# Optimization experiments

Measured on AMD Instinct MI355X. Metric: run time of the kernel, lower is better.

The kernel has to match this reference:

```python
import jax, jax.numpy as jnp
import numpy as np

N = 100000   # nodes
E = 1600000  # edges (avg degree 16)
F_IN = 50    # dataset.num_features
C = 32       # dataset.num_classes == hidden == out channels


def setup_inputs() -> dict:
    key = jax.random.key(0)
    ks = jax.random.split(key, 12)
    x = jax.random.normal(ks[0], (N, F_IN), dtype=jnp.float32)
    edge_index = jax.random.randint(ks[1], (2, E), 0, N, dtype=jnp.int64)
    dims = [(F_IN, C), (C, C), (C, C)]
    inp = {"x": x, "edge_index": edge_index}
    for i, (din, dout) in enumerate(dims, start=1):
        s = 1.0 / np.sqrt(din)
        inp[f"Wl{i}"] = jax.random.uniform(ks[2 + 3 * (i - 1)], (din, dout), jnp.float32, -s, s)
        inp[f"bl{i}"] = jax.random.uniform(ks[3 + 3 * (i - 1)], (dout,), jnp.float32, -s, s)
        inp[f"Wr{i}"] = jax.random.uniform(ks[4 + 3 * (i - 1)], (din, dout), jnp.float32, -s, s)
    return inp


def _sage_conv(x, src, dst, Wl, bl, Wr):
    # message = x[src]; scatter-max into dst; lin_l(agg) + lin_r(x)
    msg = x[src]                                      # [E, d_in]
    agg = jax.ops.segment_max(msg, dst, num_segments=N)
    agg = jnp.where(jnp.isfinite(agg), agg, jnp.zeros((), agg.dtype))  # empty segments -> 0
    return agg @ Wl + bl + x @ Wr


def reference(x, edge_index, Wl1, bl1, Wr1, Wl2, bl2, Wr2, Wl3, bl3, Wr3):
    src, dst = edge_index[0], edge_index[1]
    h = jax.nn.relu(_sage_conv(x, src, dst, Wl1, bl1, Wr1))
    h = jax.nn.relu(_sage_conv(h, src, dst, Wl2, bl2, Wr2))
    h = _sage_conv(h, src, dst, Wl3, bl3, Wr3)
    return jax.nn.log_softmax(h, axis=1)
```

## Files before the change

### kernel.cpp

```cpp
#include <hip/hip_runtime.h>
#include <math.h>

#define NN 100000
#define CD 32
#define NPB 4

#define B1N ((NN + 255) >> 8)
#define EPB_A 2048

typedef unsigned int   uint32;
typedef unsigned short ushort16;

__device__ __forceinline__ ushort16 f2b(float f) {
    uint32 u = __float_as_uint(f);
    u = (u + 0x7FFFu + ((u >> 16) & 1u)) >> 16;
    return (ushort16)u;
}
__device__ __forceinline__ float b2f_lo(uint32 u) { return __uint_as_float(u << 16); }
__device__ __forceinline__ float b2f_hi(uint32 u) { return __uint_as_float(u & 0xFFFF0000u); }

__device__ __forceinline__ uint32 pkmax(uint32 a, uint32 b) {
    uint32 d;
    asm("v_pk_max_u16 %0, %1, %2" : "=v"(d) : "v"(a), "v"(b));
    return d;
}
__device__ __forceinline__ uint32 key16(float f) {
    uint32 b = (uint32)f2b(f);
    return b ^ ((__float_as_uint(f) >> 31) ? 0xFFFFu : 0x8000u);
}
__device__ __forceinline__ uint32 dec_pk(uint32 k) {
    uint32 m = (~k >> 15) & 0x00010001u;
    uint32 X = 0x80008000u | ((m << 15) - m);
    return k ^ X;
}

__device__ __forceinline__ int edge_is64(const void* edge) {
    const long long* p = (const long long*)edge;
    int lane = threadIdx.x & 63;
    int bad = 0;
    for (int i = lane; i < 512; i += 64) {
        long long v = p[i];
        if (v < 0 || v >= NN) bad = 1;
    }
    unsigned long long anybad = __ballot(bad);
    return (anybad == 0ULL) ? 1 : 0;
}

__device__ __forceinline__ int load_idx(const void* edge, int i, int is64) {
    if (is64) return (int)((const long long*)edge)[i];
    return ((const int*)edge)[i];
}

__global__ __launch_bounds__(256) void cvt_hist_kernel(const float* __restrict__ x,
                                                       uint32* __restrict__ xb,
                                                       const void* edge, int E,
                                                       int* __restrict__ hist,
                                                       int nblkA) {
    __shared__ int lh[B1N];
    const int t = threadIdx.x;
    if ((int)blockIdx.x < nblkA) {
        const int is64 = edge_is64(edge);
        for (int b = t; b < B1N; b += 256) lh[b] = 0;
        __syncthreads();
        const int e0 = blockIdx.x * EPB_A + t;
#pragma unroll
        for (int k = 0; k < 8; ++k) {
            int e = e0 + k * 256;
            if (e < E) {
                int d = load_idx(edge, E + e, is64);
                atomicAdd(&lh[d >> 8], 1);
            }
        }
        __syncthreads();
        int* gh = hist + (size_t)blockIdx.x * B1N;
        for (int b = t; b < B1N; b += 256) gh[b] = lh[b];
    } else {
        const int tt = (blockIdx.x - nblkA) * 256 + t;
        if (tt >= NN * 32) return;
        const int n = tt >> 5;
        const int c = tt & 31;
        if (c >= 25) { xb[tt] = 0; return; }
        float2 v = *(const float2*)&x[n * 50 + 2 * c];
        xb[tt] = key16(v.x) | (key16(v.y) << 16);
    }
}

__global__ __launch_bounds__(256) void scanA_kernel(int* __restrict__ hist,
                                                    int nblk,
                                                    int* __restrict__ binTotal) {
    __shared__ int ts[256];
    const int bin = blockIdx.x;
    const int t = threadIdx.x;
    const int base = t * 4;
    int v0 = (base + 0 < nblk) ? hist[(size_t)(base + 0) * B1N + bin] : 0;
    int v1 = (base + 1 < nblk) ? hist[(size_t)(base + 1) * B1N + bin] : 0;
    int v2 = (base + 2 < nblk) ? hist[(size_t)(base + 2) * B1N + bin] : 0;
    int v3 = (base + 3 < nblk) ? hist[(size_t)(base + 3) * B1N + bin] : 0;
    const int s = v0 + v1 + v2 + v3;
    ts[t] = s;
    __syncthreads();
    for (int off = 1; off < 256; off <<= 1) {
        int u = (t >= off) ? ts[t - off] : 0;
        __syncthreads();
        ts[t] += u;
        __syncthreads();
    }
    int e = ts[t] - s;
    if (base + 0 < nblk) { hist[(size_t)(base + 0) * B1N + bin] = e; e += v0; }
    if (base + 1 < nblk) { hist[(size_t)(base + 1) * B1N + bin] = e; e += v1; }
    if (base + 2 < nblk) { hist[(size_t)(base + 2) * B1N + bin] = e; e += v2; }
    if (base + 3 < nblk) { hist[(size_t)(base + 3) * B1N + bin] = e; e += v3; }
    if (t == 255) binTotal[bin] = ts[255];
}

__device__ __forceinline__ void scan_bins_lds(const int* __restrict__ binTotal,
                                              int* ts, int* lbase) {
    const int t = threadIdx.x;
    const int base = t * 2;
    const int v0 = (base + 0 < B1N) ? binTotal[base + 0] : 0;
    const int v1 = (base + 1 < B1N) ? binTotal[base + 1] : 0;
    const int s = v0 + v1;
    ts[t] = s;
    __syncthreads();
    for (int off = 1; off < 256; off <<= 1) {
        int u = (t >= off) ? ts[t - off] : 0;
        __syncthreads();
        ts[t] += u;
        __syncthreads();
    }
    const int e = ts[t] - s;
    if (base + 0 < B1N) lbase[base + 0] = e;
    if (base + 1 < B1N) lbase[base + 1] = e + v0;
    if (t == 255) lbase[B1N] = ts[255];
    __syncthreads();
}

__global__ __launch_bounds__(256) void scatter_kernel(const void* edge, int E,
                                                      const int* __restrict__ hist,
                                                      const int* __restrict__ binTotal,
                                                      uint32* __restrict__ bucketed) {
    __shared__ int ts[256];
    __shared__ int lbase[B1N + 1];
    __shared__ int cur[B1N];
    const int is64 = edge_is64(edge);
    const int t = threadIdx.x;
    scan_bins_lds(binTotal, ts, lbase);
    const int* gh = hist + (size_t)blockIdx.x * B1N;
    for (int b = t; b < B1N; b += 256) cur[b] = lbase[b] + gh[b];
    __syncthreads();
    const int e0 = blockIdx.x * EPB_A + t;
#pragma unroll
    for (int k = 0; k < 8; ++k) {
        int e = e0 + k * 256;
        if (e < E) {
            int s = load_idx(edge, e, is64);
            int d = load_idx(edge, E + e, is64);
            int pos = atomicAdd(&cur[d >> 8], 1);
            bucketed[pos] = (uint32)s | ((uint32)(d & 255) << 17);
        }
    }
}

__global__ __launch_bounds__(256) void bucket_kernel(const uint32* __restrict__ bucketed,
                                                     const int* __restrict__ binTotal,
                                                     int* __restrict__ offsets,
                                                     int* __restrict__ csr_src) {
    __shared__ int ts[256];
    __shared__ int lbase[B1N + 1];
    __shared__ int h[256];
    __shared__ int sc[256];
    __shared__ int cur[256];
    const int bkt = blockIdx.x;
    const int t = threadIdx.x;
    scan_bins_lds(binTotal, ts, lbase);
    const int start = lbase[bkt];
    const int end   = lbase[bkt + 1];
    h[t] = 0;
    __syncthreads();
    for (int i = start + t; i < end; i += 256)
        atomicAdd(&h[bucketed[i] >> 17], 1);
    __syncthreads();
    const int v = h[t];
    sc[t] = v;
    __syncthreads();
    for (int off = 1; off < 256; off <<= 1) {
        int u = (t >= off) ? sc[t - off] : 0;
        __syncthreads();
        sc[t] += u;
        __syncthreads();
    }
    const int excl = sc[t] - v;
    const int node = bkt * 256 + t;
    if (node < NN) offsets[node] = start + excl;
    cur[t] = start + excl;
    __syncthreads();
    for (int i = start + t; i < end; i += 256) {
        uint32 p = bucketed[i];
        int pos = atomicAdd(&cur[p >> 17], 1);
        csr_src[pos] = (int)(p & 0x1FFFFu);
    }
    if (bkt == B1N - 1 && t == 0) offsets[NN] = end;
}


__global__ void gather50_kernel(const uint32* __restrict__ hb,
                                const int* __restrict__ offsets,
                                const int* __restrict__ csr_src,
                                uint32* __restrict__ aggB) {
    const int tid  = threadIdx.x;
    const int g    = tid >> 6;
    const int lane = tid & 63;
    const int p    = lane >> 5;
    const int j    = lane & 31;
    const int n    = blockIdx.x * NPB + g;
    if (n >= NN) return;

    const int beg = offsets[n];
    const int end = offsets[n + 1];
    const char* hbase = (const char*)hb;
    const uint32 joff = (uint32)(j << 2);
    const int lb = p << 5;

    uint32 a_[8];
#pragma unroll
    for (int k = 0; k < 8; ++k) a_[k] = 0;

    for (int ib = beg; ib < end; ib += 64) {
        const int rem = end - ib;
        const int mm  = rem < 64 ? rem : 64;
        const int myidx = 2 * j + p;
        int sidx = 0;
        if (myidx < mm) sidx = csr_src[ib + myidx];
        int k = p;
        for (; k + 14 < mm; k += 16) {
            const int kh = lb + (k >> 1);
#pragma unroll
            for (int kk = 0; kk < 8; ++kk) {
                int s = __shfl(sidx, kh + kk);
                uint32 u = *(const uint32*)(hbase + ((((uint32)s) << 7) | joff));
                a_[kk] = pkmax(a_[kk], u);
            }
        }
        for (; k + 6 < mm; k += 8) {
            const int kh = lb + (k >> 1);
#pragma unroll
            for (int kk = 0; kk < 4; ++kk) {
                int s = __shfl(sidx, kh + kk);
                uint32 u = *(const uint32*)(hbase + ((((uint32)s) << 7) | joff));
                a_[kk] = pkmax(a_[kk], u);
            }
        }
        for (; k < mm; k += 2) {
            int s = __shfl(sidx, lb + (k >> 1));
            uint32 u = *(const uint32*)(hbase + ((((uint32)s) << 7) | joff));
            a_[0] = pkmax(a_[0], u);
        }
    }
#pragma unroll
    for (int off2 = 4; off2 > 0; off2 >>= 1)
#pragma unroll
        for (int k = 0; k < off2; ++k)
            a_[k] = pkmax(a_[k], a_[k + off2]);
    uint32 r = a_[0];
    r = pkmax(r, (uint32)__shfl_xor((int)r, 32));
    if (p == 0 && j < 25) {
        aggB[(size_t)n * 32 + j] = (beg == end) ? 0x80008000u : r;
    }
}

__global__ void gather32_kernel(const uint32* __restrict__ hb,
                                const int* __restrict__ offsets,
                                const int* __restrict__ csr_src,
                                uint32* __restrict__ aggB) {
    const int tid  = threadIdx.x;
    const int g    = tid >> 6;
    const int lane = tid & 63;
    const int e    = lane >> 4;
    const int c    = lane & 15;
    const int n    = blockIdx.x * NPB + g;
    if (n >= NN) return;

    const int beg = offsets[n];
    const int end = offsets[n + 1];
    const char* hbase = (const char*)hb;
    const uint32 coff = (uint32)(c << 2);
    const int lb = e << 4;

    uint32 a0 = 0, a1 = 0, a2 = 0, a3 = 0;

    for (int ib = beg; ib < end; ib += 64) {
        const int rem = end - ib;
        const int mm  = rem < 64 ? rem : 64;
        const int myidx = 4 * c + e;
        int sidx = 0;
        if (myidx < mm) sidx = csr_src[ib + myidx];
        int k = e;
        for (; k + 12 < mm; k += 16) {
            const int m = lb + (k >> 2);
            int s0 = __shfl(sidx, m);
            int s1 = __shfl(sidx, m + 1);
            int s2 = __shfl(sidx, m + 2);
            int s3 = __shfl(sidx, m + 3);
            uint32 u0 = *(const uint32*)(hbase + ((((uint32)s0) << 6) | coff));
            uint32 u1 = *(const uint32*)(hbase + ((((uint32)s1) << 6) | coff));
            uint32 u2 = *(const uint32*)(hbase + ((((uint32)s2) << 6) | coff));
            uint32 u3 = *(const uint32*)(hbase + ((((uint32)s3) << 6) | coff));
            a0 = pkmax(a0, u0); a1 = pkmax(a1, u1);
            a2 = pkmax(a2, u2); a3 = pkmax(a3, u3);
        }
        for (; k < mm; k += 4) {
            int s = __shfl(sidx, lb + (k >> 2));
            uint32 u = *(const uint32*)(hbase + ((((uint32)s) << 6) | coff));
            a0 = pkmax(a0, u);
        }
    }
    uint32 r = pkmax(pkmax(a0, a1), pkmax(a2, a3));
    r = pkmax(r, (uint32)__shfl_xor((int)r, 16));
    r = pkmax(r, (uint32)__shfl_xor((int)r, 32));
    if (lane < 16) {
        aggB[(size_t)n * 16 + lane] = (beg == end) ? 0x80008000u : r;
    }
}

template <int DIN, int ASTR, int HSTR, int OSTR, int MODE>
__global__ void dense_kernel(const uint32* __restrict__ aggB,
                             const uint32* __restrict__ hB,
                             const float* __restrict__ Wl,
                             const float* __restrict__ bl,
                             const float* __restrict__ Wr,
                             void* __restrict__ out_v) {
    const int n = blockIdx.x * blockDim.x + threadIdx.x;
    if (n >= NN) return;

    float acc[CD];
#pragma unroll
    for (int j = 0; j < CD; ++j) acc[j] = bl[j];

    {
        const uint32* row = aggB + (size_t)n * ASTR;
        for (int c = 0; c < DIN / 4; ++c) {
            uint2 u = *(const uint2*)&row[c * 2];
            u.x = dec_pk(u.x); u.y = dec_pk(u.y);
            float d0 = b2f_lo(u.x), d1 = b2f_hi(u.x);
            float d2 = b2f_lo(u.y), d3 = b2f_hi(u.y);
            const float* w = Wl + c * 4 * CD;
#pragma unroll
            for (int j = 0; j < CD; ++j)
                acc[j] += d0 * w[j] + d1 * w[CD + j] + d2 * w[2 * CD + j] + d3 * w[3 * CD + j];
        }
        if (DIN % 4) {
            uint32 u = dec_pk(row[(DIN / 4) * 2]);
            float d0 = b2f_lo(u), d1 = b2f_hi(u);
            const float* w = Wl + (DIN - 2) * CD;
#pragma unroll
            for (int j = 0; j < CD; ++j)
                acc[j] += d0 * w[j] + d1 * w[CD + j];
        }
    }
    {
        const uint32* row = hB + (size_t)n * HSTR;
        for (int c = 0; c < DIN / 4; ++c) {
            uint2 u = *(const uint2*)&row[c * 2];
            u.x = dec_pk(u.x); u.y = dec_pk(u.y);
            float d0 = b2f_lo(u.x), d1 = b2f_hi(u.x);
            float d2 = b2f_lo(u.y), d3 = b2f_hi(u.y);
            const float* w = Wr + c * 4 * CD;
#pragma unroll
            for (int j = 0; j < CD; ++j)
                acc[j] += d0 * w[j] + d1 * w[CD + j] + d2 * w[2 * CD + j] + d3 * w[3 * CD + j];
        }
        if (DIN % 4) {
            uint32 u = dec_pk(row[(DIN / 4) * 2]);
            float d0 = b2f_lo(u), d1 = b2f_hi(u);
            const float* w = Wr + (DIN - 2) * CD;
#pragma unroll
            for (int j = 0; j < CD; ++j)
                acc[j] += d0 * w[j] + d1 * w[CD + j];
        }
    }

    if (MODE == 0) {
        uint32* orow = (uint32*)out_v + (size_t)n * OSTR;
#pragma unroll
        for (int c = 0; c < CD / 2; ++c) {
            float a0 = fmaxf(acc[2 * c],     0.0f);
            float a1 = fmaxf(acc[2 * c + 1], 0.0f);
            orow[c] = ((uint32)f2b(a0) | ((uint32)f2b(a1) << 16)) | 0x80008000u;
        }
    } else {
        float m = acc[0];
#pragma unroll
        for (int j = 1; j < CD; ++j) m = fmaxf(m, acc[j]);
        float s = 0.0f;
#pragma unroll
        for (int j = 0; j < CD; ++j) s += expf(acc[j] - m);
        const float lse = m + logf(s);
        float* orow = (float*)out_v + (size_t)n * CD;
#pragma unroll
        for (int j = 0; j < CD; ++j) orow[j] = acc[j] - lse;
    }
}

extern "C" void kernel_launch(void* const* d_in, const int* in_sizes, int n_in,
                              void* d_out, int out_size, void* d_ws, size_t ws_size,
                              hipStream_t stream) {
    const float* x    = (const float*)d_in[0];
    const void*  edge = d_in[1];
    const float* Wl1 = (const float*)d_in[2];
    const float* bl1 = (const float*)d_in[3];
    const float* Wr1 = (const float*)d_in[4];
    const float* Wl2 = (const float*)d_in[5];
    const float* bl2 = (const float*)d_in[6];
    const float* Wr2 = (const float*)d_in[7];
    const float* Wl3 = (const float*)d_in[8];
    const float* bl3 = (const float*)d_in[9];
    const float* Wr3 = (const float*)d_in[10];

    const int E = in_sizes[1] / 2;

    char* ws = (char*)d_ws;
    size_t off = 0;
    auto carve = [&](size_t bytes) {
        void* p = ws + off;
        off = (off + bytes + 255) & ~(size_t)255;
        return p;
    };
    int*    offsets   = (int*)   carve((size_t)(NN + 1) * 4);
    int*    binTotal  = (int*)   carve((size_t)B1N * 4);
    int*    csr_src   = (int*)   carve((size_t)E * 4);
    uint32* xb        = (uint32*)carve((size_t)NN * 32 * 4);
    uint32* h1b       = (uint32*)carve((size_t)NN * 16 * 4);
    (void)ws_size; (void)n_in; (void)out_size;

    uint32* bucketed = (uint32*)d_out;
    int*    hist     = (int*)((char*)d_out + (((size_t)E * 4 + 255) & ~(size_t)255));
    uint32* agg1 = (uint32*)d_out;
    uint32* agg2 = (uint32*)d_out;
    uint32* h2b  = xb;
    uint32* agg3 = h1b;

    const int nblkA = (E + EPB_A - 1) / EPB_A;
    const int cvtb  = (NN * 32 + 255) / 256;
    cvt_hist_kernel<<<nblkA + cvtb, 256, 0, stream>>>(x, xb, edge, E, hist, nblkA);
    scanA_kernel<<<B1N, 256, 0, stream>>>(hist, nblkA, binTotal);
    scatter_kernel<<<nblkA, 256, 0, stream>>>(edge, E, hist, binTotal, bucketed);
    bucket_kernel<<<B1N, 256, 0, stream>>>(bucketed, binTotal, offsets, csr_src);

    const int gb = (NN + NPB - 1) / NPB;
    const int db = (NN + 255) / 256;

    gather50_kernel<<<gb, 256, 0, stream>>>(xb, offsets, csr_src, agg1);
    dense_kernel<50, 32, 32, 16, 0><<<db, 256, 0, stream>>>(agg1, xb, Wl1, bl1, Wr1, h1b);
    gather32_kernel<<<gb, 256, 0, stream>>>(h1b, offsets, csr_src, agg2);
    dense_kernel<32, 16, 16, 16, 0><<<db, 256, 0, stream>>>(agg2, h1b, Wl2, bl2, Wr2, h2b);
    gather32_kernel<<<gb, 256, 0, stream>>>(h2b, offsets, csr_src, agg3);
    dense_kernel<32, 16, 16, 0, 2><<<db, 256, 0, stream>>>(agg3, h2b, Wl3, bl3, Wr3, d_out);
}
```

Baseline: 302.7 us.

## Split layer-1 features into column-partitioned tables and batch nodes per wave in gathers

The 50-wide bf16 input is repacked into three 16-column planes plus a separate 2-column tail. Layer-1 gather runs in three passes, one per plane, each reading 32-byte rows so a pass's table is smaller and caches better. A new dense50 kernel reads the split layout. Both gather kernels now process four nodes per wave with their index loads issued up front, giving more memory-level parallelism. The cost is more launched blocks and more register use per wave.

```diff
diff --git a/kernel.cpp b/kernel.cpp
--- a/kernel.cpp
+++ b/kernel.cpp
@@ -4,6 +4,8 @@
 #define NN 100000
 #define CD 32
 #define NPB 4
+#define G50_NPW 4
+#define G32_NPW 4
 
 #define B1N ((NN + 255) >> 8)
 #define EPB_A 2048
@@ -52,7 +54,8 @@
 }
 
 __global__ __launch_bounds__(256) void cvt_hist_kernel(const float* __restrict__ x,
-                                                       uint32* __restrict__ xb,
+                                                       uint32* __restrict__ xc,
+                                                       uint32* __restrict__ xc3,
                                                        const void* edge, int E,
                                                        int* __restrict__ hist,
                                                        int nblkA) {
@@ -76,12 +79,19 @@
         for (int b = t; b < B1N; b += 256) gh[b] = lh[b];
     } else {
         const int tt = (blockIdx.x - nblkA) * 256 + t;
-        if (tt >= NN * 32) return;
-        const int n = tt >> 5;
-        const int c = tt & 31;
-        if (c >= 25) { xb[tt] = 0; return; }
-        float2 v = *(const float2*)&x[n * 50 + 2 * c];
-        xb[tt] = key16(v.x) | (key16(v.y) << 16);
+        if (tt < NN * 24) {
+            const int p  = tt / (NN * 8);
+            const int r  = tt - p * NN * 8;
+            const int n  = r >> 3;
+            const int cc = r & 7;
+            const int u  = 8 * p + cc;
+            float2 v = *(const float2*)&x[n * 50 + 2 * u];
+            xc[tt] = key16(v.x) | (key16(v.y) << 16);
+        } else if (tt < NN * 24 + NN) {
+            const int n = tt - NN * 24;
+            float2 v = *(const float2*)&x[n * 50 + 48];
+            xc3[n] = key16(v.x) | (key16(v.y) << 16);
+        }
     }
 }
 
@@ -203,68 +213,113 @@
 }
 
 
-__global__ void gather50_kernel(const uint32* __restrict__ hb,
+__global__ void gather50_kernel(const uint32* __restrict__ xc,
+                                const uint32* __restrict__ xc3,
                                 const int* __restrict__ offsets,
                                 const int* __restrict__ csr_src,
-                                uint32* __restrict__ aggB) {
+                                uint32* __restrict__ aggp,
+                                uint32* __restrict__ agg24,
+                                int gb) {
     const int tid  = threadIdx.x;
     const int g    = tid >> 6;
     const int lane = tid & 63;
-    const int p    = lane >> 5;
-    const int j    = lane & 31;
-    const int n    = blockIdx.x * NPB + g;
-    if (n >= NN) return;
-
-    const int beg = offsets[n];
-    const int end = offsets[n + 1];
-    const char* hbase = (const char*)hb;
-    const uint32 joff = (uint32)(j << 2);
-    const int lb = p << 5;
-
-    uint32 a_[8];
-#pragma unroll
-    for (int k = 0; k < 8; ++k) a_[k] = 0;
-
-    for (int ib = beg; ib < end; ib += 64) {
-        const int rem = end - ib;
-        const int mm  = rem < 64 ? rem : 64;
-        const int myidx = 2 * j + p;
-        int sidx = 0;
-        if (myidx < mm) sidx = csr_src[ib + myidx];
-        int k = p;
-        for (; k + 14 < mm; k += 16) {
-            const int kh = lb + (k >> 1);
-#pragma unroll
-            for (int kk = 0; kk < 8; ++kk) {
-                int s = __shfl(sidx, kh + kk);
-                uint32 u = *(const uint32*)(hbase + ((((uint32)s) << 7) | joff));
-                a_[kk] = pkmax(a_[kk], u);
+    const int e    = lane & 7;
+    const int c    = lane >> 3;
+    const int pass = blockIdx.x / gb;
+    const int blk  = blockIdx.x - pass * gb;
+    const int n0   = (blk * NPB + g) * G50_NPW;
+    if (n0 >= NN) return;
+    const bool p0 = (pass == 0);
+
+    const char* tb = (const char*)(xc + (size_t)pass * NN * 8);
+    const uint32 coff = (uint32)(c << 2);
+
+    int beg[G50_NPW], end[G50_NPW], mm[G50_NPW], sidx[G50_NPW];
+#pragma unroll
+    for (int q = 0; q < G50_NPW; ++q) {
+        const int n = n0 + q;
+        const bool ok = (n < NN);
+        beg[q] = ok ? offsets[n] : 0;
+        end[q] = ok ? offsets[n + 1] : 0;
+        int d = end[q] - beg[q];
+        mm[q] = d < 64 ? d : 64;
+    }
+#pragma unroll
+    for (int q = 0; q < G50_NPW; ++q)
+        sidx[q] = (lane < mm[q]) ? csr_src[beg[q] + lane] : 0;
+
+    uint32 acc[G50_NPW], a24[G50_NPW];
+#pragma unroll
+    for (int q = 0; q < G50_NPW; ++q) { acc[q] = 0; a24[q] = 0; }
+
+#pragma unroll
+    for (int q = 0; q < G50_NPW; ++q) {
+        for (int k = e; k < mm[q]; k += 8) {
+            int s = __shfl(sidx[q], k);
+            acc[q] = pkmax(acc[q], *(const uint32*)(tb + ((((uint32)s) << 5) | coff)));
+        }
+        if (p0 && lane < mm[q]) a24[q] = pkmax(a24[q], xc3[sidx[q]]);
+    }
+#pragma unroll
+    for (int q = 0; q < G50_NPW; ++q) {
+        for (int ib = beg[q] + 64; ib < end[q]; ib += 64) {
+            const int rem = end[q] - ib;
+            const int m = rem < 64 ? rem : 64;
+            int sx = (lane < m) ? csr_src[ib + lane] : 0;
+            for (int k = e; k < m; k += 8) {
+                int s = __shfl(sx, k);
+                acc[q] = pkmax(acc[q], *(const uint32*)(tb + ((((uint32)s) << 5) | coff)));
             }
-        }
-        for (; k + 6 < mm; k += 8) {
-            const int kh = lb + (k >> 1);
-#pragma unroll
-            for (int kk = 0; kk < 4; ++kk) {
-                int s = __shfl(sidx, kh + kk);
-                uint32 u = *(const uint32*)(hbase + ((((uint32)s) << 7) | joff));
-                a_[kk] = pkmax(a_[kk], u);
-            }
-        }
-        for (; k < mm; k += 2) {
-            int s = __shfl(sidx, lb + (k >> 1));
-            uint32 u = *(const uint32*)(hbase + ((((uint32)s) << 7) | joff));
-            a_[0] = pkmax(a_[0], u);
-        }
-    }
-#pragma unroll
-    for (int off2 = 4; off2 > 0; off2 >>= 1)
-#pragma unroll
-        for (int k = 0; k < off2; ++k)
-            a_[k] = pkmax(a_[k], a_[k + off2]);
-    uint32 r = a_[0];
-    r = pkmax(r, (uint32)__shfl_xor((int)r, 32));
-    if (p == 0 && j < 25) {
-        aggB[(size_t)n * 32 + j] = (beg == end) ? 0x80008000u : r;
+            if (p0 && lane < m) a24[q] = pkmax(a24[q], xc3[sx]);
+        }
+    }
+
+#pragma unroll
+    for (int q = 0; q < G50_NPW; ++q) {
+        const int n = n0 + q;
+        uint32 r = acc[q];
+        r = pkmax(r, (uint32)__shfl_xor((int)r, 1));
+        r = pkmax(r, (uint32)__shfl_xor((int)r, 2));
+        r = pkmax(r, (uint32)__shfl_xor((int)r, 4));
+        if (e == 0 && n < NN) {
+            aggp[((size_t)pass * NN + n) * 8 + c] =
+                (beg[q] == end[q]) ? 0x80008000u : r;
+        }
+        if (p0) {
+            uint32 s24 = a24[q];
+            s24 = pkmax(s24, (uint32)__shfl_xor((int)s24, 1));
+            s24 = pkmax(s24, (uint32)__shfl_xor((int)s24, 2));
+            s24 = pkmax(s24, (uint32)__shfl_xor((int)s24, 4));
+            s24 = pkmax(s24, (uint32)__shfl_xor((int)s24, 8));
+            s24 = pkmax(s24, (uint32)__shfl_xor((int)s24, 16));
+            s24 = pkmax(s24, (uint32)__shfl_xor((int)s24, 32));
+            if (lane == 0 && n < NN)
+                agg24[n] = (beg[q] == end[q]) ? 0x80008000u : s24;
+        }
+    }
+}
+
+__device__ __forceinline__ void g32_window(uint32* a_, int sidx, int mm,
+                                           const char* hbase, uint32 coff,
+                                           int e, int lb) {
+    int k = e;
+    for (; k + 12 < mm; k += 16) {
+        const int m = lb + (k >> 2);
+        int s0 = __shfl(sidx, m);
+        int s1 = __shfl(sidx, m + 1);
+        int s2 = __shfl(sidx, m + 2);
+        int s3 = __shfl(sidx, m + 3);
+        uint32 u0 = *(const uint32*)(hbase + ((((uint32)s0) << 6) | coff));
+        uint32 u1 = *(const uint32*)(hbase + ((((uint32)s1) << 6) | coff));
+        uint32 u2 = *(const uint32*)(hbase + ((((uint32)s2) << 6) | coff));
+        uint32 u3 = *(const uint32*)(hbase + ((((uint32)s3) << 6) | coff));
+        a_[0] = pkmax(a_[0], u0); a_[1] = pkmax(a_[1], u1);
+        a_[2] = pkmax(a_[2], u2); a_[3] = pkmax(a_[3], u3);
+    }
+    for (; k < mm; k += 4) {
+        int s = __shfl(sidx, lb + (k >> 2));
+        uint32 u = *(const uint32*)(hbase + ((((uint32)s) << 6) | coff));
+        a_[0] = pkmax(a_[0], u);
     }
 }
 
@@ -277,48 +332,109 @@
     const int lane = tid & 63;
     const int e    = lane >> 4;
     const int c    = lane & 15;
-    const int n    = blockIdx.x * NPB + g;
-    if (n >= NN) return;
-
-    const int beg = offsets[n];
-    const int end = offsets[n + 1];
+    const int n0   = (blockIdx.x * NPB + g) * G32_NPW;
+    if (n0 >= NN) return;
+
     const char* hbase = (const char*)hb;
     const uint32 coff = (uint32)(c << 2);
     const int lb = e << 4;
-
-    uint32 a0 = 0, a1 = 0, a2 = 0, a3 = 0;
-
-    for (int ib = beg; ib < end; ib += 64) {
-        const int rem = end - ib;
-        const int mm  = rem < 64 ? rem : 64;
-        const int myidx = 4 * c + e;
-        int sidx = 0;
-        if (myidx < mm) sidx = csr_src[ib + myidx];
-        int k = e;
-        for (; k + 12 < mm; k += 16) {
-            const int m = lb + (k >> 2);
-            int s0 = __shfl(sidx, m);
-            int s1 = __shfl(sidx, m + 1);
-            int s2 = __shfl(sidx, m + 2);
-            int s3 = __shfl(sidx, m + 3);
-            uint32 u0 = *(const uint32*)(hbase + ((((uint32)s0) << 6) | coff));
-            uint32 u1 = *(const uint32*)(hbase + ((((uint32)s1) << 6) | coff));
-            uint32 u2 = *(const uint32*)(hbase + ((((uint32)s2) << 6) | coff));
-            uint32 u3 = *(const uint32*)(hbase + ((((uint32)s3) << 6) | coff));
-            a0 = pkmax(a0, u0); a1 = pkmax(a1, u1);
-            a2 = pkmax(a2, u2); a3 = pkmax(a3, u3);
-        }
-        for (; k < mm; k += 4) {
-            int s = __shfl(sidx, lb + (k >> 2));
-            uint32 u = *(const uint32*)(hbase + ((((uint32)s) << 6) | coff));
-            a0 = pkmax(a0, u);
-        }
-    }
-    uint32 r = pkmax(pkmax(a0, a1), pkmax(a2, a3));
-    r = pkmax(r, (uint32)__shfl_xor((int)r, 16));
-    r = pkmax(r, (uint32)__shfl_xor((int)r, 32));
-    if (lane < 16) {
-        aggB[(size_t)n * 16 + lane] = (beg == end) ? 0x80008000u : r;
+    const int myidx = 4 * c + e;
+
+    int beg[G32_NPW], end[G32_NPW], mm[G32_NPW], sidx[G32_NPW];
+#pragma unroll
+    for (int q = 0; q < G32_NPW; ++q) {
+        const int n = n0 + q;
+        const bool ok = (n < NN);
+        beg[q] = ok ? offsets[n] : 0;
+        end[q] = ok ? offsets[n + 1] : 0;
+        int d = end[q] - beg[q];
+        mm[q] = d < 64 ? d : 64;
+    }
+#pragma unroll
+    for (int q = 0; q < G32_NPW; ++q)
+        sidx[q] = (myidx < mm[q]) ? csr_src[beg[q] + myidx] : 0;
+
+    uint32 A[G32_NPW][4];
+#pragma unroll
+    for (int q = 0; q < G32_NPW; ++q)
+#pragma unroll
+        for (int k = 0; k < 4; ++k) A[q][k] = 0;
+
+#pragma unroll
+    for (int q = 0; q < G32_NPW; ++q)
+        g32_window(A[q], sidx[q], mm[q], hbase, coff, e, lb);
+#pragma unroll
+    for (int q = 0; q < G32_NPW; ++q) {
+        for (int ib = beg[q] + 64; ib < end[q]; ib += 64) {
+            const int rem = end[q] - ib;
+            const int m = rem < 64 ? rem : 64;
+            int sx = (myidx < m) ? csr_src[ib + myidx] : 0;
+            g32_window(A[q], sx, m, hbase, coff, e, lb);
+        }
+    }
+
+#pragma unroll
+    for (int q = 0; q < G32_NPW; ++q) {
+        const int n = n0 + q;
+        uint32 r = pkmax(pkmax(A[q][0], A[q][1]), pkmax(A[q][2], A[q][3]));
+        r = pkmax(r, (uint32)__shfl_xor((int)r, 16));
+        r = pkmax(r, (uint32)__shfl_xor((int)r, 32));
+        if (lane < 16 && n < NN)
+            aggB[(size_t)n * 16 + lane] = (beg[q] == end[q]) ? 0x80008000u : r;
+    }
+}
+
+__global__ void dense50_kernel(const uint32* __restrict__ aggp,
+                               const uint32* __restrict__ agg24,
+                               const uint32* __restrict__ xc,
+                               const uint32* __restrict__ xc3,
+                               const float* __restrict__ Wl,
+                               const float* __restrict__ bl,
+                               const float* __restrict__ Wr,
+                               uint32* __restrict__ out) {
+    const int n = blockIdx.x * blockDim.x + threadIdx.x;
+    if (n >= NN) return;
+
+    float acc[CD];
+#pragma unroll
+    for (int j = 0; j < CD; ++j) acc[j] = bl[j];
+
+#pragma unroll
+    for (int side = 0; side < 2; ++side) {
+        const uint32* tp = side ? xc  : aggp;
+        const uint32* t3 = side ? xc3 : agg24;
+        const float*  W  = side ? Wr  : Wl;
+#pragma unroll
+        for (int p = 0; p < 3; ++p) {
+            const uint32* row = tp + ((size_t)p * NN + n) * 8;
+#pragma unroll
+            for (int q = 0; q < 4; ++q) {
+                uint2 uu = *(const uint2*)&row[q * 2];
+                uint32 ux = dec_pk(uu.x), uy = dec_pk(uu.y);
+                float d0 = b2f_lo(ux), d1 = b2f_hi(ux);
+                float d2 = b2f_lo(uy), d3 = b2f_hi(uy);
+                const float* w = W + (p * 16 + q * 4) * CD;
+#pragma unroll
+                for (int j = 0; j < CD; ++j)
+                    acc[j] += d0 * w[j] + d1 * w[CD + j] + d2 * w[2 * CD + j] + d3 * w[3 * CD + j];
+            }
+        }
+        {
+            uint32 u = dec_pk(t3[n]);
+            float d0 = b2f_lo(u), d1 = b2f_hi(u);
+            const float* w = W + 48 * CD;
+#pragma unroll
+            for (int j = 0; j < CD; ++j)
+                acc[j] += d0 * w[j] + d1 * w[CD + j];
+        }
+    }
+
+    uint32* orow = out + (size_t)n * 16;
+#pragma unroll
+    for (int c = 0; c < CD / 2; ++c) {
+        float a0 = fmaxf(acc[2 * c],     0.0f);
+        float a1 = fmaxf(acc[2 * c + 1], 0.0f);
+        orow[c] = ((uint32)f2b(a0) | ((uint32)f2b(a1) << 16)) | 0x80008000u;
     }
 }
 
@@ -348,14 +464,6 @@
             for (int j = 0; j < CD; ++j)
                 acc[j] += d0 * w[j] + d1 * w[CD + j] + d2 * w[2 * CD + j] + d3 * w[3 * CD + j];
         }
-        if (DIN % 4) {
-            uint32 u = dec_pk(row[(DIN / 4) * 2]);
-            float d0 = b2f_lo(u), d1 = b2f_hi(u);
-            const float* w = Wl + (DIN - 2) * CD;
-#pragma unroll
-            for (int j = 0; j < CD; ++j)
-                acc[j] += d0 * w[j] + d1 * w[CD + j];
-        }
     }
     {
         const uint32* row = hB + (size_t)n * HSTR;
@@ -368,14 +476,6 @@
 #pragma unroll
             for (int j = 0; j < CD; ++j)
                 acc[j] += d0 * w[j] + d1 * w[CD + j] + d2 * w[2 * CD + j] + d3 * w[3 * CD + j];
-        }
-        if (DIN % 4) {
-            uint32 u = dec_pk(row[(DIN / 4) * 2]);
-            float d0 = b2f_lo(u), d1 = b2f_hi(u);
-            const float* w = Wr + (DIN - 2) * CD;
-#pragma unroll
-            for (int j = 0; j < CD; ++j)
-                acc[j] += d0 * w[j] + d1 * w[CD + j];
         }
     }
 
@@ -428,31 +528,35 @@
     int*    offsets   = (int*)   carve((size_t)(NN + 1) * 4);
     int*    binTotal  = (int*)   carve((size_t)B1N * 4);
     int*    csr_src   = (int*)   carve((size_t)E * 4);
-    uint32* xb        = (uint32*)carve((size_t)NN * 32 * 4);
+    uint32* xc        = (uint32*)carve((size_t)NN * 24 * 4);
+    uint32* xc3       = (uint32*)carve((size_t)NN * 4);
     uint32* h1b       = (uint32*)carve((size_t)NN * 16 * 4);
     (void)ws_size; (void)n_in; (void)out_size;
 
     uint32* bucketed = (uint32*)d_out;
     int*    hist     = (int*)((char*)d_out + (((size_t)E * 4 + 255) & ~(size_t)255));
-    uint32* agg1 = (uint32*)d_out;
+    uint32* aggp  = (uint32*)d_out;
+    uint32* agg24 = (uint32*)d_out + (size_t)NN * 24;
     uint32* agg2 = (uint32*)d_out;
-    uint32* h2b  = xb;
+    uint32* h2b  = xc;
     uint32* agg3 = h1b;
 
     const int nblkA = (E + EPB_A - 1) / EPB_A;
-    const int cvtb  = (NN * 32 + 255) / 256;
-    cvt_hist_kernel<<<nblkA + cvtb, 256, 0, stream>>>(x, xb, edge, E, hist, nblkA);
+    const int cvtb  = (NN * 25 + 255) / 256;
+    cvt_hist_kernel<<<nblkA + cvtb, 256, 0, stream>>>(x, xc, xc3, edge, E, hist, nblkA);
     scanA_kernel<<<B1N, 256, 0, stream>>>(hist, nblkA, binTotal);
     scatter_kernel<<<nblkA, 256, 0, stream>>>(edge, E, hist, binTotal, bucketed);
     bucket_kernel<<<B1N, 256, 0, stream>>>(bucketed, binTotal, offsets, csr_src);
 
-    const int gb = (NN + NPB - 1) / NPB;
-    const int db = (NN + 255) / 256;
-
-    gather50_kernel<<<gb, 256, 0, stream>>>(xb, offsets, csr_src, agg1);
-    dense_kernel<50, 32, 32, 16, 0><<<db, 256, 0, stream>>>(agg1, xb, Wl1, bl1, Wr1, h1b);
-    gather32_kernel<<<gb, 256, 0, stream>>>(h1b, offsets, csr_src, agg2);
+    const int gb50 = (NN + NPB * G50_NPW - 1) / (NPB * G50_NPW);
+    const int gb32 = (NN + NPB * G32_NPW - 1) / (NPB * G32_NPW);
+    const int db   = (NN + 255) / 256;
+
+    gather50_kernel<<<3 * gb50, 256, 0, stream>>>(xc, xc3, offsets, csr_src,
+                                                  aggp, agg24, gb50);
+    dense50_kernel<<<db, 256, 0, stream>>>(aggp, agg24, xc, xc3, Wl1, bl1, Wr1, h1b);
+    gather32_kernel<<<gb32, 256, 0, stream>>>(h1b, offsets, csr_src, agg2);
     dense_kernel<32, 16, 16, 16, 0><<<db, 256, 0, stream>>>(agg2, h1b, Wl2, bl2, Wr2, h2b);
-    gather32_kernel<<<gb, 256, 0, stream>>>(h2b, offsets, csr_src, agg3);
+    gather32_kernel<<<gb32, 256, 0, stream>>>(h2b, offsets, csr_src, agg3);
     dense_kernel<32, 16, 16, 0, 2><<<db, 256, 0, stream>>>(agg3, h2b, Wl3, bl3, Wr3, d_out);
 }
```

Measured after the change: 359.1 us. 1.19x slower.

## Process four nodes per wavefront in gather kernels to batch index loads

Applied to the files above, without the earlier changes.

Each wavefront in the gather50 and gather32 kernels now handles four destination nodes instead of one. It loads all offsets and the first window of CSR indices for the four nodes up front, then runs their gathers back to back. The aim is to hide the latency of the dependent offset and index loads and to keep more memory requests in flight per wave. In exchange the grid has four times fewer blocks and each thread holds more registers, which can lower occupancy and worsen load imbalance across nodes of different degree.

```diff
diff --git a/kernel.cpp b/kernel.cpp
--- a/kernel.cpp
+++ b/kernel.cpp
@@ -4,6 +4,7 @@
 #define NN 100000
 #define CD 32
 #define NPB 4
+#define G_NPW 4
 
 #define B1N ((NN + 255) >> 8)
 #define EPB_A 2048
@@ -203,6 +204,35 @@
 }
 
 
+__device__ __forceinline__ void g50_window(uint32* a_, int sidx, int mm,
+                                           const char* hbase, uint32 joff,
+                                           int p, int lb) {
+    int k = p;
+    for (; k + 14 < mm; k += 16) {
+        const int kh = lb + (k >> 1);
+#pragma unroll
+        for (int kk = 0; kk < 8; ++kk) {
+            int s = __shfl(sidx, kh + kk);
+            uint32 u = *(const uint32*)(hbase + ((((uint32)s) << 7) | joff));
+            a_[kk] = pkmax(a_[kk], u);
+        }
+    }
+    for (; k + 6 < mm; k += 8) {
+        const int kh = lb + (k >> 1);
+#pragma unroll
+        for (int kk = 0; kk < 4; ++kk) {
+            int s = __shfl(sidx, kh + kk);
+            uint32 u = *(const uint32*)(hbase + ((((uint32)s) << 7) | joff));
+            a_[kk] = pkmax(a_[kk], u);
+        }
+    }
+    for (; k < mm; k += 2) {
+        int s = __shfl(sidx, lb + (k >> 1));
+        uint32 u = *(const uint32*)(hbase + ((((uint32)s) << 7) | joff));
+        a_[0] = pkmax(a_[0], u);
+    }
+}
+
 __global__ void gather50_kernel(const uint32* __restrict__ hb,
                                 const int* __restrict__ offsets,
                                 const int* __restrict__ csr_src,
@@ -212,59 +242,83 @@
     const int lane = tid & 63;
     const int p    = lane >> 5;
     const int j    = lane & 31;
-    const int n    = blockIdx.x * NPB + g;
-    if (n >= NN) return;
-
-    const int beg = offsets[n];
-    const int end = offsets[n + 1];
+    const int n0   = (blockIdx.x * NPB + g) * G_NPW;
+    if (n0 >= NN) return;
+
     const char* hbase = (const char*)hb;
     const uint32 joff = (uint32)(j << 2);
     const int lb = p << 5;
-
-    uint32 a_[8];
-#pragma unroll
-    for (int k = 0; k < 8; ++k) a_[k] = 0;
-
-    for (int ib = beg; ib < end; ib += 64) {
-        const int rem = end - ib;
-        const int mm  = rem < 64 ? rem : 64;
-        const int myidx = 2 * j + p;
-        int sidx = 0;
-        if (myidx < mm) sidx = csr_src[ib + myidx];
-        int k = p;
-        for (; k + 14 < mm; k += 16) {
-            const int kh = lb + (k >> 1);
-#pragma unroll
-            for (int kk = 0; kk < 8; ++kk) {
-                int s = __shfl(sidx, kh + kk);
-                uint32 u = *(const uint32*)(hbase + ((((uint32)s) << 7) | joff));
-                a_[kk] = pkmax(a_[kk], u);
-            }
-        }
-        for (; k + 6 < mm; k += 8) {
-            const int kh = lb + (k >> 1);
-#pragma unroll
-            for (int kk = 0; kk < 4; ++kk) {
-                int s = __shfl(sidx, kh + kk);
-                uint32 u = *(const uint32*)(hbase + ((((uint32)s) << 7) | joff));
-                a_[kk] = pkmax(a_[kk], u);
-            }
-        }
-        for (; k < mm; k += 2) {
-            int s = __shfl(sidx, lb + (k >> 1));
-            uint32 u = *(const uint32*)(hbase + ((((uint32)s) << 7) | joff));
-            a_[0] = pkmax(a_[0], u);
-        }
-    }
-#pragma unroll
-    for (int off2 = 4; off2 > 0; off2 >>= 1)
-#pragma unroll
-        for (int k = 0; k < off2; ++k)
-            a_[k] = pkmax(a_[k], a_[k + off2]);
-    uint32 r = a_[0];
-    r = pkmax(r, (uint32)__shfl_xor((int)r, 32));
-    if (p == 0 && j < 25) {
-        aggB[(size_t)n * 32 + j] = (beg == end) ? 0x80008000u : r;
+    const int myidx = 2 * j + p;
+
+    int beg[G_NPW], end[G_NPW], mm[G_NPW], sidx[G_NPW];
+#pragma unroll
+    for (int q = 0; q < G_NPW; ++q) {
+        const int n = n0 + q;
+        const bool ok = (n < NN);
+        beg[q] = ok ? offsets[n] : 0;
+        end[q] = ok ? offsets[n + 1] : 0;
+        int d = end[q] - beg[q];
+        mm[q] = d < 64 ? d : 64;
+    }
+#pragma unroll
+    for (int q = 0; q < G_NPW; ++q)
+        sidx[q] = (myidx < mm[q]) ? csr_src[beg[q] + myidx] : 0;
+
+    uint32 A[G_NPW][8];
+#pragma unroll
+    for (int q = 0; q < G_NPW; ++q)
+#pragma unroll
+        for (int k = 0; k < 8; ++k) A[q][k] = 0;
+
+#pragma unroll
+    for (int q = 0; q < G_NPW; ++q)
+        g50_window(A[q], sidx[q], mm[q], hbase, joff, p, lb);
+#pragma unroll
+    for (int q = 0; q < G_NPW; ++q) {
+        for (int ib = beg[q] + 64; ib < end[q]; ib += 64) {
+            const int rem = end[q] - ib;
+            const int m = rem < 64 ? rem : 64;
+            int sx = (myidx < m) ? csr_src[ib + myidx] : 0;
+            g50_window(A[q], sx, m, hbase, joff, p, lb);
+        }
+    }
+
+#pragma unroll
+    for (int q = 0; q < G_NPW; ++q) {
+        const int n = n0 + q;
+#pragma unroll
+        for (int off2 = 4; off2 > 0; off2 >>= 1)
+#pragma unroll
+            for (int k = 0; k < off2; ++k)
+                A[q][k] = pkmax(A[q][k], A[q][k + off2]);
+        uint32 r = A[q][0];
+        r = pkmax(r, (uint32)__shfl_xor((int)r, 32));
+        if (p == 0 && j < 25 && n < NN)
+            aggB[(size_t)n * 32 + j] = (beg[q] == end[q]) ? 0x80008000u : r;
+    }
+}
+
+__device__ __forceinline__ void g32_window(uint32* a_, int sidx, int mm,
+                                           const char* hbase, uint32 coff,
+                                           int e, int lb) {
+    int k = e;
+    for (; k + 12 < mm; k += 16) {
+        const int m = lb + (k >> 2);
+        int s0 = __shfl(sidx, m);
+        int s1 = __shfl(sidx, m + 1);
+        int s2 = __shfl(sidx, m + 2);
+        int s3 = __shfl(sidx, m + 3);
+        uint32 u0 = *(const uint32*)(hbase + ((((uint32)s0) << 6) | coff));
+        uint32 u1 = *(const uint32*)(hbase + ((((uint32)s1) << 6) | coff));
+        uint32 u2 = *(const uint32*)(hbase + ((((uint32)s2) << 6) | coff));
+        uint32 u3 = *(const uint32*)(hbase + ((((uint32)s3) << 6) | coff));
+        a_[0] = pkmax(a_[0], u0); a_[1] = pkmax(a_[1], u1);
+        a_[2] = pkmax(a_[2], u2); a_[3] = pkmax(a_[3], u3);
+    }
+    for (; k < mm; k += 4) {
+        int s = __shfl(sidx, lb + (k >> 2));
+        uint32 u = *(const uint32*)(hbase + ((((uint32)s) << 6) | coff));
+        a_[0] = pkmax(a_[0], u);
     }
 }
 
@@ -277,48 +331,55 @@
     const int lane = tid & 63;
     const int e    = lane >> 4;
     const int c    = lane & 15;
-    const int n    = blockIdx.x * NPB + g;
-    if (n >= NN) return;
-
-    const int beg = offsets[n];
-    const int end = offsets[n + 1];
+    const int n0   = (blockIdx.x * NPB + g) * G_NPW;
+    if (n0 >= NN) return;
+
     const char* hbase = (const char*)hb;
     const uint32 coff = (uint32)(c << 2);
     const int lb = e << 4;
-
-    uint32 a0 = 0, a1 = 0, a2 = 0, a3 = 0;
-
-    for (int ib = beg; ib < end; ib += 64) {
-        const int rem = end - ib;
-        const int mm  = rem < 64 ? rem : 64;
-        const int myidx = 4 * c + e;
-        int sidx = 0;
-        if (myidx < mm) sidx = csr_src[ib + myidx];
-        int k = e;
-        for (; k + 12 < mm; k += 16) {
-            const int m = lb + (k >> 2);
-            int s0 = __shfl(sidx, m);
-            int s1 = __shfl(sidx, m + 1);
-            int s2 = __shfl(sidx, m + 2);
-            int s3 = __shfl(sidx, m + 3);
-            uint32 u0 = *(const uint32*)(hbase + ((((uint32)s0) << 6) | coff));
-            uint32 u1 = *(const uint32*)(hbase + ((((uint32)s1) << 6) | coff));
-            uint32 u2 = *(const uint32*)(hbase + ((((uint32)s2) << 6) | coff));
-            uint32 u3 = *(const uint32*)(hbase + ((((uint32)s3) << 6) | coff));
-            a0 = pkmax(a0, u0); a1 = pkmax(a1, u1);
-            a2 = pkmax(a2, u2); a3 = pkmax(a3, u3);
-        }
-        for (; k < mm; k += 4) {
-            int s = __shfl(sidx, lb + (k >> 2));
-            uint32 u = *(const uint32*)(hbase + ((((uint32)s) << 6) | coff));
-            a0 = pkmax(a0, u);
-        }
-    }
-    uint32 r = pkmax(pkmax(a0, a1), pkmax(a2, a3));
-    r = pkmax(r, (uint32)__shfl_xor((int)r, 16));
-    r = pkmax(r, (uint32)__shfl_xor((int)r, 32));
-    if (lane < 16) {
-        aggB[(size_t)n * 16 + lane] = (beg == end) ? 0x80008000u : r;
+    const int myidx = 4 * c + e;
+
+    int beg[G_NPW], end[G_NPW], mm[G_NPW], sidx[G_NPW];
+#pragma unroll
+    for (int q = 0; q < G_NPW; ++q) {
+        const int n = n0 + q;
+        const bool ok = (n < NN);
+        beg[q] = ok ? offsets[n] : 0;
+        end[q] = ok ? offsets[n + 1] : 0;
+        int d = end[q] - beg[q];
+        mm[q] = d < 64 ? d : 64;
+    }
+#pragma unroll
+    for (int q = 0; q < G_NPW; ++q)
+        sidx[q] = (myidx < mm[q]) ? csr_src[beg[q] + myidx] : 0;
+
+    uint32 A[G_NPW][4];
+#pragma unroll
+    for (int q = 0; q < G_NPW; ++q)
+#pragma unroll
+        for (int k = 0; k < 4; ++k) A[q][k] = 0;
+
+#pragma unroll
+    for (int q = 0; q < G_NPW; ++q)
+        g32_window(A[q], sidx[q], mm[q], hbase, coff, e, lb);
+#pragma unroll
+    for (int q = 0; q < G_NPW; ++q) {
+        for (int ib = beg[q] + 64; ib < end[q]; ib += 64) {
+            const int rem = end[q] - ib;
+            const int m = rem < 64 ? rem : 64;
+            int sx = (myidx < m) ? csr_src[ib + myidx] : 0;
+            g32_window(A[q], sx, m, hbase, coff, e, lb);
+        }
+    }
+
+#pragma unroll
+    for (int q = 0; q < G_NPW; ++q) {
+        const int n = n0 + q;
+        uint32 r = pkmax(pkmax(A[q][0], A[q][1]), pkmax(A[q][2], A[q][3]));
+        r = pkmax(r, (uint32)__shfl_xor((int)r, 16));
+        r = pkmax(r, (uint32)__shfl_xor((int)r, 32));
+        if (lane < 16 && n < NN)
+            aggB[(size_t)n * 16 + lane] = (beg[q] == end[q]) ? 0x80008000u : r;
     }
 }
 
@@ -446,7 +507,7 @@
     scatter_kernel<<<nblkA, 256, 0, stream>>>(edge, E, hist, binTotal, bucketed);
     bucket_kernel<<<B1N, 256, 0, stream>>>(bucketed, binTotal, offsets, csr_src);
 
-    const int gb = (NN + NPB - 1) / NPB;
+    const int gb = (NN + NPB * G_NPW - 1) / (NPB * G_NPW);
     const int db = (NN + 255) / 256;
 
     gather50_kernel<<<gb, 256, 0, stream>>>(xb, offsets, csr_src, agg1);
```

New measurement: 294.0 us. 1.03x faster.
